# Performance work log

Measured on AMD Instinct MI355X. Metric: run time of the kernel, lower is better.

Reference implementation:

```python
import jax, jax.numpy as jnp
import numpy as np

N_ITEMS = 200_000
N_USERS = 50_000
EMB = 100
BATCH = 100
HIST_MAX = 50
LAYERS = 3
NNZ_A = 6_400_000
NNZ_H = 25_000


def setup_inputs() -> dict:
    key = jax.random.key(0)
    ks = jax.random.split(key, 12)
    return dict(
        adj_row=jax.random.randint(ks[0], (NNZ_A,), 0, N_ITEMS, dtype=jnp.int32),
        adj_col=jax.random.randint(ks[1], (NNZ_A,), 0, N_ITEMS, dtype=jnp.int32),
        adj_val=jax.random.uniform(ks[2], (NNZ_A,), dtype=jnp.float32),
        hist_row=jax.random.randint(ks[3], (NNZ_H,), 0, BATCH * HIST_MAX, dtype=jnp.int32),
        hist_col=jax.random.randint(ks[4], (NNZ_H,), 0, N_ITEMS, dtype=jnp.int32),
        hist_val=jax.random.uniform(ks[5], (NNZ_H,), dtype=jnp.float32),
        hist_len=jax.random.randint(ks[6], (BATCH,), 0, HIST_MAX, dtype=jnp.int32),
        user=jax.random.randint(ks[7], (BATCH,), 0, N_USERS, dtype=jnp.int32),
        embedding=jax.random.normal(ks[8], (N_ITEMS, EMB), dtype=jnp.float32),
        user_embedding=jax.random.normal(ks[9], (N_USERS, EMB), dtype=jnp.float32),
        gamma_k=jax.random.uniform(ks[10], (LAYERS + 1,), dtype=jnp.float32),
        W_1=jax.random.normal(ks[11], (2 * EMB, 1), dtype=jnp.float32),
    )


def spmm(row, col, val, x, n_rows):
    # COO sparse @ dense: gather rows of x by col, scale, scatter-add by row.
    return jax.ops.segment_sum(val[:, None] * x[col], row, num_segments=n_rows)


def reference(adj_row, adj_col, adj_val, hist_row, hist_col, hist_val,
              hist_len, user, embedding, user_embedding, gamma_k, W_1):
    # Multi-layer hypergraph propagation with gamma-weighted accumulation.
    item = embedding
    acc = embedding * gamma_k[0]
    for i in range(LAYERS):
        item = spmm(adj_row, adj_col, adj_val, item, N_ITEMS) * gamma_k[i + 1]
        acc = acc + item
    item_embeddings = acc  # [N_ITEMS, EMB]

    # ishist=True branch: attention-masked history aggregation.
    ue = user_embedding[user]  # [B, E]
    hist_emb = spmm(hist_row, hist_col, hist_val, item_embeddings,
                    BATCH * HIST_MAX).reshape(BATCH, HIST_MAX, EMB)
    mask = jnp.arange(HIST_MAX, dtype=hist_len.dtype)[None, :] >= hist_len[:, None]
    neg = mask.astype(item_embeddings.dtype) * (-99999.0)
    # cat(query_user, hist_emb) @ W_1 == ue @ W_1[:E] + hist_emb @ W_1[E:]
    alpha = (ue @ W_1[:EMB, 0])[:, None] + jnp.einsum('bhe,e->bh', hist_emb, W_1[EMB:, 0]) + neg
    alpha = jax.nn.softmax(alpha, axis=1)  # [B, H]
    denom = jnp.where(hist_len == 0, 1, hist_len).astype(item_embeddings.dtype)
    user_out = jnp.sum(alpha[:, :, None] * hist_emb, axis=1) / denom[:, None]  # [B, E]
    return (item_embeddings, user_out)
```

## Files before the change

kernel.cpp:

```cpp
#include <hip/hip_runtime.h>
#include <hip/hip_fp16.h>

#define EMB 100
#define EMB4 25
#define SLOTS 13
#define PADH 104
#define N_ITEMS 200000
#define BATCH 100
#define HIST_MAX 50
#define ITEM_ELEMS 20000000
#define SCAN_B 1024
#define NSCAN_BLOCKS ((N_ITEMS + SCAN_B - 1) / SCAN_B)
#define VALQ 16383.0f

typedef unsigned int u32;


__global__ void k_histogram(const int* __restrict__ row, int* __restrict__ cnt, int nnz) {
    int i = blockIdx.x * blockDim.x + threadIdx.x;
    if (i < nnz) atomicAdd(&cnt[row[i]], 1);
}

__global__ void k_scan_local(const int* __restrict__ cnt, int* __restrict__ rowptr,
                             int* __restrict__ blocksum, int n) {
    __shared__ int sd[SCAN_B];
    int b = blockIdx.x, tid = threadIdx.x;
    int i = b * SCAN_B + tid;
    int v = (i < n) ? cnt[i] : 0;
    sd[tid] = v;
    __syncthreads();
    for (int off = 1; off < SCAN_B; off <<= 1) {
        int t = (tid >= off) ? sd[tid - off] : 0;
        __syncthreads();
        sd[tid] += t;
        __syncthreads();
    }
    if (i < n) rowptr[i + 1] = sd[tid];
    if (tid == SCAN_B - 1) blocksum[b] = sd[tid];
}

__global__ void k_scan_blocks(int* __restrict__ blocksum, int nb) {
    __shared__ int sd[256];
    int tid = threadIdx.x;
    int v = (tid < nb) ? blocksum[tid] : 0;
    sd[tid] = v;
    __syncthreads();
    for (int off = 1; off < 256; off <<= 1) {
        int t = (tid >= off) ? sd[tid - off] : 0;
        __syncthreads();
        sd[tid] += t;
        __syncthreads();
    }
    if (tid < nb) blocksum[tid] = sd[tid] - v;
}

__global__ void k_scan_add(int* __restrict__ rowptr, const int* __restrict__ blocksum, int n) {
    int i = blockIdx.x * blockDim.x + threadIdx.x;
    if (i == 0) rowptr[0] = 0;
    if (i < n) rowptr[i + 1] += blocksum[i / SCAN_B];
}

__global__ void k_fill(const int* __restrict__ row, const int* __restrict__ col,
                       const float* __restrict__ val, const int* __restrict__ rowptr,
                       int* __restrict__ cnt, u32* __restrict__ cvp, int nnz) {
    int i = blockIdx.x * blockDim.x + threadIdx.x;
    if (i >= nnz) return;
    int r = row[i];
    int old = atomicSub(&cnt[r], 1);
    int pos = rowptr[r] + old - 1;
    u32 q = (u32)__float2uint_rn(val[i] * VALQ);
    cvp[pos] = ((u32)col[i] << 14) | q;
}

__global__ void k_to_half(const float* __restrict__ src, __half* __restrict__ dst) {
    int t = blockIdx.x * blockDim.x + threadIdx.x;
    if (t >= N_ITEMS * SLOTS) return;
    int r = t / SLOTS;
    int sl = t - r * SLOTS;
    int e0 = sl * 8;
    const float* s = src + r * EMB;
    __half h[8];
#pragma unroll
    for (int k = 0; k < 8; k++) {
        int e = e0 + k;
        h[k] = __float2half((e < EMB) ? s[e] : 0.f);
    }
    *(uint4*)(dst + r * PADH + e0) = *(const uint4*)h;
}


__device__ __forceinline__ void fma8(float s[8], const uint4& hv, float f) {
    const __half2* hp = reinterpret_cast<const __half2*>(&hv);
#pragma unroll
    for (int k = 0; k < 4; k++) {
        float2 p = __half22float2(hp[k]);
        s[2 * k]     += f * p.x;
        s[2 * k + 1] += f * p.y;
    }
}

__global__ void k_spmm_gather_h(const int* __restrict__ rowptr, const u32* __restrict__ cvp,
                                const __half* __restrict__ x,
                                const float* __restrict__ gamma, int gidx,
                                __half* __restrict__ outh,
                                const float* __restrict__ emb,
                                const __half* __restrict__ h1, const __half* __restrict__ h2,
                                float* __restrict__ acc) {
    int t = blockIdx.x * blockDim.x + threadIdx.x;
    if (t >= N_ITEMS * SLOTS) return;
    int r = t / SLOTS;
    int sl = t - r * SLOTS;
    int e0 = sl * 8;
    int j0 = rowptr[r], j1 = rowptr[r + 1];
    const float inv = 1.0f / VALQ;
    float s[8] = {0.f, 0.f, 0.f, 0.f, 0.f, 0.f, 0.f, 0.f};
    int j = j0;
    for (; j + 4 <= j1; j += 4) {
        u32 w0 = cvp[j + 0];
        u32 w1 = cvp[j + 1];
        u32 w2 = cvp[j + 2];
        u32 w3 = cvp[j + 3];
        uint4 v0 = *(const uint4*)(x + (w0 >> 14) * PADH + e0);
        uint4 v1 = *(const uint4*)(x + (w1 >> 14) * PADH + e0);
        uint4 v2 = *(const uint4*)(x + (w2 >> 14) * PADH + e0);
        uint4 v3 = *(const uint4*)(x + (w3 >> 14) * PADH + e0);
        fma8(s, v0, (float)(w0 & 16383u) * inv);
        fma8(s, v1, (float)(w1 & 16383u) * inv);
        fma8(s, v2, (float)(w2 & 16383u) * inv);
        fma8(s, v3, (float)(w3 & 16383u) * inv);
    }
    for (; j < j1; ++j) {
        u32 w = cvp[j];
        uint4 v = *(const uint4*)(x + (w >> 14) * PADH + e0);
        fma8(s, v, (float)(w & 16383u) * inv);
    }
    float g = gamma[gidx];
#pragma unroll
    for (int k = 0; k < 8; k++) s[k] *= g;

    if (acc) {
        float g0 = gamma[0];
        uint4 a = *(const uint4*)(h1 + r * PADH + e0);
        uint4 b = *(const uint4*)(h2 + r * PADH + e0);
        const __half2* ap = reinterpret_cast<const __half2*>(&a);
        const __half2* bp = reinterpret_cast<const __half2*>(&b);
        float o[8];
#pragma unroll
        for (int k = 0; k < 4; k++) {
            float2 pa = __half22float2(ap[k]);
            float2 pb = __half22float2(bp[k]);
            o[2 * k]     = s[2 * k]     + pa.x + pb.x;
            o[2 * k + 1] = s[2 * k + 1] + pa.y + pb.y;
        }
        const float* ep = emb + r * EMB + e0;
        float* op = acc + r * EMB + e0;
        float4 e1v = *(const float4*)(ep);
        float4 w1v = make_float4(o[0] + g0 * e1v.x, o[1] + g0 * e1v.y,
                                 o[2] + g0 * e1v.z, o[3] + g0 * e1v.w);
        *(float4*)(op) = w1v;
        if (e0 + 8 <= EMB) {
            float4 e2v = *(const float4*)(ep + 4);
            float4 w2v = make_float4(o[4] + g0 * e2v.x, o[5] + g0 * e2v.y,
                                     o[6] + g0 * e2v.z, o[7] + g0 * e2v.w);
            *(float4*)(op + 4) = w2v;
        }
    } else {
        __half hh[8];
#pragma unroll
        for (int k = 0; k < 8; k++) hh[k] = __float2half(s[k]);
        *(uint4*)(outh + r * PADH + e0) = *(const uint4*)hh;
    }
}


__global__ void k_init_acc(const float* __restrict__ emb,
                           const float* __restrict__ gamma,
                           float* __restrict__ acc, int n4) {
    int t = blockIdx.x * blockDim.x + threadIdx.x;
    if (t >= n4) return;
    float g = gamma[0];
    float4 v = ((const float4*)emb)[t];
    v.x *= g; v.y *= g; v.z *= g; v.w *= g;
    ((float4*)acc)[t] = v;
}

__global__ void k_acc_add(float* __restrict__ acc,
                          const float* __restrict__ item, int n4) {
    int t = blockIdx.x * blockDim.x + threadIdx.x;
    if (t >= n4) return;
    float4 a = ((float4*)acc)[t];
    float4 b = ((const float4*)item)[t];
    a.x += b.x; a.y += b.y; a.z += b.z; a.w += b.w;
    ((float4*)acc)[t] = a;
}

__global__ void k_spmm_atomic(const int* __restrict__ row,
                              const int* __restrict__ col,
                              const float* __restrict__ val,
                              const float* __restrict__ gamma, int gidx,
                              const float* __restrict__ x,
                              float* __restrict__ out, int nnz) {
    long long t = (long long)blockIdx.x * blockDim.x + threadIdx.x;
    long long total = (long long)nnz * EMB4;
    if (t >= total) return;
    int n = (int)(t / EMB4);
    int q = (int)(t % EMB4);
    int r = row[n];
    int c = col[n];
    float s = (gidx >= 0) ? gamma[gidx] : 1.0f;
    float v = val[n] * s;
    float4 xv = ((const float4*)x)[c * EMB4 + q];
    float* o = out + (long long)r * EMB + q * 4;
    atomicAdd(o + 0, v * xv.x);
    atomicAdd(o + 1, v * xv.y);
    atomicAdd(o + 2, v * xv.z);
    atomicAdd(o + 3, v * xv.w);
}

__global__ void k_attn(const float* __restrict__ hist_emb,
                       const int* __restrict__ hist_len,
                       const int* __restrict__ user,
                       const float* __restrict__ user_emb,
                       const float* __restrict__ W1,
                       float* __restrict__ out_user) {
    __shared__ float w[2 * EMB];
    __shared__ float he[HIST_MAX * EMB];
    __shared__ float alpha[HIST_MAX];
    __shared__ float ued, mx, sm;
    int b = blockIdx.x;
    int tid = threadIdx.x;

    for (int i = tid; i < 2 * EMB; i += blockDim.x) w[i] = W1[i];
    for (int i = tid; i < HIST_MAX * EMB; i += blockDim.x)
        he[i] = hist_emb[(long long)b * HIST_MAX * EMB + i];
    __syncthreads();

    if (tid == 0) {
        const float* ue = user_emb + (long long)user[b] * EMB;
        float s = 0.f;
        for (int e = 0; e < EMB; e++) s += ue[e] * w[e];
        ued = s;
    }
    __syncthreads();

    int len = hist_len[b];
    if (tid < HIST_MAX) {
        float d = 0.f;
        for (int e = 0; e < EMB; e++) d += he[tid * EMB + e] * w[EMB + e];
        alpha[tid] = ued + d + (tid >= len ? -99999.0f : 0.0f);
    }
    __syncthreads();

    if (tid == 0) {
        float m = -1e30f;
        for (int h = 0; h < HIST_MAX; h++) m = fmaxf(m, alpha[h]);
        mx = m;
    }
    __syncthreads();
    if (tid < HIST_MAX) alpha[tid] = expf(alpha[tid] - mx);
    __syncthreads();
    if (tid == 0) {
        float s = 0.f;
        for (int h = 0; h < HIST_MAX; h++) s += alpha[h];
        sm = s;
    }
    __syncthreads();

    float denom = (len == 0) ? 1.0f : (float)len;
    if (tid < EMB) {
        float s = 0.f;
        for (int h = 0; h < HIST_MAX; h++) s += alpha[h] * he[h * EMB + tid];
        out_user[(long long)b * EMB + tid] = s / (sm * denom);
    }
}

extern "C" void kernel_launch(void* const* d_in, const int* in_sizes, int n_in,
                              void* d_out, int out_size, void* d_ws, size_t ws_size,
                              hipStream_t stream) {
    const int*   adj_row  = (const int*)d_in[0];
    const int*   adj_col  = (const int*)d_in[1];
    const float* adj_val  = (const float*)d_in[2];
    const int*   hist_row = (const int*)d_in[3];
    const int*   hist_col = (const int*)d_in[4];
    const float* hist_val = (const float*)d_in[5];
    const int*   hist_len = (const int*)d_in[6];
    const int*   user     = (const int*)d_in[7];
    const float* embedding      = (const float*)d_in[8];
    const float* user_embedding = (const float*)d_in[9];
    const float* gamma    = (const float*)d_in[10];
    const float* W1       = (const float*)d_in[11];

    float* acc      = (float*)d_out;
    float* user_out = acc + ITEM_ELEMS;

    int nnzA = in_sizes[0];
    int nnzH = in_sizes[3];

    const size_t HBT = (size_t)N_ITEMS * PADH * sizeof(__half);
    char* ws = (char*)d_ws;
    __half* hb0 = (__half*)(ws + 0 * HBT);
    __half* hb1 = (__half*)(ws + 1 * HBT);
    __half* hb2 = (__half*)(ws + 2 * HBT);
    float*  buf1 = (float*)(ws + 0);
    float*  buf2 = (float*)(ws + 80000000ULL);
    size_t off = 3 * HBT;
    u32*   cvp  = (u32*)(ws + off);       off += (size_t)nnzA * 4;
    int*   rowptr = (int*)(ws + off);     off += ((size_t)N_ITEMS + 4) * 4;
    int*   cnt  = (int*)(ws + off);       off += (size_t)N_ITEMS * 4;
    int*   blocksum = (int*)(ws + off);   off += 256 * 4;
    float* histe = (float*)(ws + off);    off += (size_t)BATCH * HIST_MAX * EMB * 4;
    size_t need_csr = off;

    const int n4 = ITEM_ELEMS / 4;
    long long totH = (long long)nnzH * EMB4;
    int blocksH = (int)((totH + 255) / 256);

    if (ws_size >= need_csr) {
        hipMemsetAsync(cnt, 0, (size_t)N_ITEMS * 4, stream);
        hipMemsetAsync(histe, 0, (size_t)BATCH * HIST_MAX * EMB * 4, stream);

        int bN = (nnzA + 255) / 256;
        k_histogram<<<bN, 256, 0, stream>>>(adj_row, cnt, nnzA);
        k_scan_local<<<NSCAN_BLOCKS, SCAN_B, 0, stream>>>(cnt, rowptr, blocksum, N_ITEMS);
        k_scan_blocks<<<1, 256, 0, stream>>>(blocksum, NSCAN_BLOCKS);
        k_scan_add<<<(N_ITEMS + 255) / 256, 256, 0, stream>>>(rowptr, blocksum, N_ITEMS);
        k_fill<<<bN, 256, 0, stream>>>(adj_row, adj_col, adj_val, rowptr, cnt, cvp, nnzA);

        int gThreads = N_ITEMS * SLOTS;
        int gBlocks = (gThreads + 255) / 256;
        k_to_half<<<gBlocks, 256, 0, stream>>>(embedding, hb0);
        k_spmm_gather_h<<<gBlocks, 256, 0, stream>>>(rowptr, cvp, hb0, gamma, 1,
                                                     hb1, nullptr, nullptr, nullptr, nullptr);
        k_spmm_gather_h<<<gBlocks, 256, 0, stream>>>(rowptr, cvp, hb1, gamma, 2,
                                                     hb2, nullptr, nullptr, nullptr, nullptr);
        k_spmm_gather_h<<<gBlocks, 256, 0, stream>>>(rowptr, cvp, hb2, gamma, 3,
                                                     nullptr, embedding, hb1, hb2, acc);
    } else {
        hipMemsetAsync(buf1, 0, 80000000ULL, stream);
        hipMemsetAsync(buf2, 0, 80000000ULL, stream);
        hipMemsetAsync(histe, 0, (size_t)BATCH * HIST_MAX * EMB * 4, stream);

        k_init_acc<<<(n4 + 255) / 256, 256, 0, stream>>>(embedding, gamma, acc, n4);
        long long totA = (long long)nnzA * EMB4;
        int blocksA = (int)((totA + 255) / 256);
        k_spmm_atomic<<<blocksA, 256, 0, stream>>>(adj_row, adj_col, adj_val, gamma, 1,
                                                   embedding, buf1, nnzA);
        k_acc_add<<<(n4 + 255) / 256, 256, 0, stream>>>(acc, buf1, n4);
        k_spmm_atomic<<<blocksA, 256, 0, stream>>>(adj_row, adj_col, adj_val, gamma, 2,
                                                   buf1, buf2, nnzA);
        k_acc_add<<<(n4 + 255) / 256, 256, 0, stream>>>(acc, buf2, n4);
        k_spmm_atomic<<<blocksA, 256, 0, stream>>>(adj_row, adj_col, adj_val, gamma, 3,
                                                   buf2, acc, nnzA);
    }

    k_spmm_atomic<<<blocksH, 256, 0, stream>>>(hist_row, hist_col, hist_val, gamma, -1,
                                               acc, histe, nnzH);

    k_attn<<<BATCH, 128, 0, stream>>>(histe, hist_len, user, user_embedding, W1, user_out);
}
```

Measured before the change: 1.734 ms.

## Replace atomic COO-to-CSR fill with two-pass binned counting sort

The original fill kernel scattered each nonzero straight to its CSR slot, using a global atomic per element and writing to random addresses. The new path first counts nonzeros per 1024-row bin in each 8192-element chunk and scans those counts. It then scatters 64-bit packed entries into contiguous bin regions with shared-memory atomics, and a per-bin pass places each entry at its final row position using shared-memory cursors. This trades random global atomics and scattered writes for extra kernel launches, an additional scan, and an extra pass over an 8-byte staging buffer that reuses the hb1 workspace.

```diff
diff --git a/kernel.cpp b/kernel.cpp
--- a/kernel.cpp
+++ b/kernel.cpp
@@ -13,7 +13,13 @@
 #define NSCAN_BLOCKS ((N_ITEMS + SCAN_B - 1) / SCAN_B)
 #define VALQ 16383.0f
 
+#define ENT 8192
+#define BIN_SHIFT 10
+#define ROWS_PER_BIN 1024
+#define NBINS ((N_ITEMS + ROWS_PER_BIN - 1) >> BIN_SHIFT)
+
 typedef unsigned int u32;
+typedef unsigned long long u64;
 
 
 __global__ void k_histogram(const int* __restrict__ row, int* __restrict__ cnt, int nnz) {
@@ -60,16 +66,63 @@
     if (i < n) rowptr[i + 1] += blocksum[i / SCAN_B];
 }
 
-__global__ void k_fill(const int* __restrict__ row, const int* __restrict__ col,
-                       const float* __restrict__ val, const int* __restrict__ rowptr,
-                       int* __restrict__ cnt, u32* __restrict__ cvp, int nnz) {
-    int i = blockIdx.x * blockDim.x + threadIdx.x;
-    if (i >= nnz) return;
-    int r = row[i];
-    int old = atomicSub(&cnt[r], 1);
-    int pos = rowptr[r] + old - 1;
-    u32 q = (u32)__float2uint_rn(val[i] * VALQ);
-    cvp[pos] = ((u32)col[i] << 14) | q;
+__global__ __launch_bounds__(256)
+void k_countbins(const int* __restrict__ row, int nnz, int nblk,
+                 int* __restrict__ counts) {
+    __shared__ int h[NBINS];
+    int blk = blockIdx.x;
+    for (int b = threadIdx.x; b < NBINS; b += 256) h[b] = 0;
+    __syncthreads();
+    int i0 = blk * ENT;
+    int i1 = i0 + ENT; if (i1 > nnz) i1 = nnz;
+    for (int i = i0 + threadIdx.x; i < i1; i += 256)
+        atomicAdd(&h[row[i] >> BIN_SHIFT], 1);
+    __syncthreads();
+    for (int b = threadIdx.x; b < NBINS; b += 256)
+        counts[b * nblk + blk] = h[b];
+}
+
+__global__ __launch_bounds__(256)
+void k_binfill(const int* __restrict__ row, const int* __restrict__ col,
+               const float* __restrict__ val, const int* __restrict__ offs,
+               int nnz, int nblk, u64* __restrict__ stage) {
+    __shared__ int base[NBINS];
+    __shared__ int h[NBINS];
+    int blk = blockIdx.x;
+    for (int b = threadIdx.x; b < NBINS; b += 256) {
+        base[b] = offs[b * nblk + blk];
+        h[b] = 0;
+    }
+    __syncthreads();
+    int i0 = blk * ENT;
+    int i1 = i0 + ENT; if (i1 > nnz) i1 = nnz;
+    for (int i = i0 + threadIdx.x; i < i1; i += 256) {
+        int r = row[i];
+        int b = r >> BIN_SHIFT;
+        int rank = atomicAdd(&h[b], 1);
+        u32 q = (u32)__float2uint_rn(val[i] * VALQ);
+        u32 cv = ((u32)col[i] << 14) | q;
+        stage[base[b] + rank] = ((u64)(u32)(r & (ROWS_PER_BIN - 1)) << 32) | cv;
+    }
+}
+
+__global__ __launch_bounds__(512)
+void k_place2(const u64* __restrict__ stage, const int* __restrict__ rowptr,
+              u32* __restrict__ cvp) {
+    __shared__ int cur[ROWS_PER_BIN];
+    int b = blockIdx.x;
+    int r0 = b << BIN_SHIFT;
+    int rend = r0 + ROWS_PER_BIN; if (rend > N_ITEMS) rend = N_ITEMS;
+    int nr = rend - r0;
+    for (int i = threadIdx.x; i < nr; i += 512) cur[i] = rowptr[r0 + i];
+    __syncthreads();
+    int jb = rowptr[r0], je = rowptr[rend];
+    for (int j = jb + threadIdx.x; j < je; j += 512) {
+        u64 e = stage[j];
+        int rl = (int)(e >> 32);
+        int pos = atomicAdd(&cur[rl], 1);
+        cvp[pos] = (u32)e;
+    }
 }
 
 __global__ void k_to_half(const float* __restrict__ src, __half* __restrict__ dst) {
@@ -296,11 +349,16 @@
     int nnzA = in_sizes[0];
     int nnzH = in_sizes[3];
 
+    int nblk = (nnzA + ENT - 1) / ENT;
+    int countsN = NBINS * nblk;
+    int nsb = (countsN + SCAN_B - 1) / SCAN_B;
+
     const size_t HBT = (size_t)N_ITEMS * PADH * sizeof(__half);
     char* ws = (char*)d_ws;
     __half* hb0 = (__half*)(ws + 0 * HBT);
     __half* hb1 = (__half*)(ws + 1 * HBT);
     __half* hb2 = (__half*)(ws + 2 * HBT);
+    u64*    stage = (u64*)(ws + 1 * HBT);
     float*  buf1 = (float*)(ws + 0);
     float*  buf2 = (float*)(ws + 80000000ULL);
     size_t off = 3 * HBT;
@@ -308,8 +366,13 @@
     int*   rowptr = (int*)(ws + off);     off += ((size_t)N_ITEMS + 4) * 4;
     int*   cnt  = (int*)(ws + off);       off += (size_t)N_ITEMS * 4;
     int*   blocksum = (int*)(ws + off);   off += 256 * 4;
+    int*   blocksum2 = (int*)(ws + off);  off += 256 * 4;
+    int*   counts = (int*)(ws + off);     off += (size_t)countsN * 4;
+    int*   offs = (int*)(ws + off);       off += ((size_t)countsN + 8) * 4;
     float* histe = (float*)(ws + off);    off += (size_t)BATCH * HIST_MAX * EMB * 4;
     size_t need_csr = off;
+    if ((size_t)nnzA * 8 > 2 * HBT) need_csr = (size_t)1 << 62;
+    if (nsb > 256) need_csr = (size_t)1 << 62;
 
     const int n4 = ITEM_ELEMS / 4;
     long long totH = (long long)nnzH * EMB4;
@@ -324,7 +387,12 @@
         k_scan_local<<<NSCAN_BLOCKS, SCAN_B, 0, stream>>>(cnt, rowptr, blocksum, N_ITEMS);
         k_scan_blocks<<<1, 256, 0, stream>>>(blocksum, NSCAN_BLOCKS);
         k_scan_add<<<(N_ITEMS + 255) / 256, 256, 0, stream>>>(rowptr, blocksum, N_ITEMS);
-        k_fill<<<bN, 256, 0, stream>>>(adj_row, adj_col, adj_val, rowptr, cnt, cvp, nnzA);
+        k_countbins<<<nblk, 256, 0, stream>>>(adj_row, nnzA, nblk, counts);
+        k_scan_local<<<nsb, SCAN_B, 0, stream>>>(counts, offs, blocksum2, countsN);
+        k_scan_blocks<<<1, 256, 0, stream>>>(blocksum2, nsb);
+        k_scan_add<<<(countsN + 255) / 256, 256, 0, stream>>>(offs, blocksum2, countsN);
+        k_binfill<<<nblk, 256, 0, stream>>>(adj_row, adj_col, adj_val, offs, nnzA, nblk, stage);
+        k_place2<<<NBINS, 512, 0, stream>>>(stage, rowptr, cvp);
 
         int gThreads = N_ITEMS * SLOTS;
         int gBlocks = (gThreads + 255) / 256;
```

After: 1.584 ms. 8.7% less time.
